# Kernel tuning notes

Hardware: AMD Instinct MI355X
Metric: run time of the kernel (lower is better)

Reference implementation:

```python
import jax, jax.numpy as jnp
import numpy as np

B, T = 4, 2048
IN_DIM = 128          # eff_in_dim == eff_out_dim (n_groups = 1)
IN_POINTS = 32
OUT_POINTS = 32
QUERY_DIM = 256
OUT_QUERY_DIM = 256
HIDDEN = QUERY_DIM // 4                       # 64
CHANNEL_PARAMS = IN_DIM * IN_DIM              # 16384
SPATIAL_PARAMS = OUT_POINTS * IN_POINTS       # 1024
TOTAL_PARAMS = CHANNEL_PARAMS + SPATIAL_PARAMS  # 17408
LN_EPS = 1e-6


def setup_inputs() -> dict:
    key = jax.random.key(0)
    ks = jax.random.split(key, 10)
    inp = {
        "sampled": jax.random.normal(ks[0], (B, T, 1, IN_POINTS, IN_DIM), jnp.float32),
        "query": jax.random.normal(ks[1], (B, T, QUERY_DIM), jnp.float32),
        # parameter_generator: LayerNorm(QUERY_DIM) -> Linear(QUERY_DIM, HIDDEN) -> Linear(HIDDEN, TOTAL_PARAMS)
        "ln_w": jnp.ones((QUERY_DIM,), jnp.float32) * QUERY_DIM ** -0.5,
        "ln_b": jnp.zeros((QUERY_DIM,), jnp.float32),
        "w1": jax.random.normal(ks[2], (HIDDEN, QUERY_DIM), jnp.float32) * 0.05,
        "b1": jax.random.normal(ks[3], (HIDDEN,), jnp.float32) * 0.02,
        "w2": jax.random.normal(ks[4], (TOTAL_PARAMS, HIDDEN), jnp.float32) * 0.05,
        "b2": jax.random.normal(ks[5], (TOTAL_PARAMS,), jnp.float32) * 0.05,
        "m_beta": jnp.zeros((IN_DIM,), jnp.float32),
        "s_beta": jnp.zeros((OUT_POINTS,), jnp.float32),
        "wo": jax.random.normal(ks[6], (OUT_QUERY_DIM, IN_DIM * OUT_POINTS), jnp.float32) * 0.02,
        "bo": jax.random.normal(ks[7], (OUT_QUERY_DIM,), jnp.float32) * 0.02,
    }
    return inp


def reference(sampled, query, ln_w, ln_b, w1, b1, w2, b2, m_beta, s_beta, wo, bo):
    b, t, g, P, C = sampled.shape  # g == 1
    BT = b * t
    OP = s_beta.shape[0]

    # parameter generator: LN -> Linear -> Linear (no activation in between)
    mu = jnp.mean(query, axis=-1, keepdims=True)
    var = jnp.var(query, axis=-1, keepdims=True)
    q = (query - mu) * jax.lax.rsqrt(var + LN_EPS) * ln_w + ln_b
    h = q @ w1.T + b1                               # [B, T, HIDDEN]
    params = (h @ w2.T + b2).reshape(BT, -1)        # [BT, TOTAL_PARAMS]

    channel_mixing = params[:, : C * C].reshape(BT, C, C)      # [BT, C, C]
    spatial_mixing = params[:, C * C :].reshape(BT, OP, P)     # [BT, OP, P]

    x = sampled.reshape(BT, P, C)
    # channel mixing: baddbmm(m_beta, x, channel_mixing) then GELU (exact/erf)
    x = jax.nn.gelu(jnp.einsum("bpc,bcd->bpd", x, channel_mixing) + m_beta,
                    approximate=False)
    # spatial mixing: baddbmm(s_beta, spatial_mixing, x) then GELU
    x = jax.nn.gelu(jnp.einsum("bop,bpd->bod", spatial_mixing, x) + s_beta[:, None],
                    approximate=False)

    out = x.reshape(b, t, -1) @ wo.T + bo           # [B, T, OUT_QUERY_DIM]
    return out
```

## Files before the change

kernel.cpp:

```cpp
#include <hip/hip_runtime.h>
#include <cstdint>


typedef __bf16 bf16x8 __attribute__((ext_vector_type(8)));
typedef float  f32x4  __attribute__((ext_vector_type(4)));
typedef unsigned short ushort;
typedef ushort ushort8 __attribute__((ext_vector_type(8)));

#define TW 16

__device__ __forceinline__ ushort f2b(float f) {
    union { float f; uint32_t u; } v; v.f = f;
    uint32_t u = v.u;
    u += 0x7fffu + ((u >> 16) & 1u);
    return (ushort)(u >> 16);
}
__device__ __forceinline__ uint32_t pk2(float a, float b) {
    return (uint32_t)f2b(a) | ((uint32_t)f2b(b) << 16);
}
__device__ __forceinline__ float gelu_fast(float x) {
    float z = fabsf(x) * 0.70710678118654752440f;
    float t = __builtin_amdgcn_rcpf(fmaf(0.3275911f, z, 1.0f));
    float p = t * fmaf(t, fmaf(t, fmaf(t, fmaf(t, 1.061405429f, -1.453152027f),
                                       1.421413741f), -0.284496736f), 0.254829592f);
    float e = __expf(-z * z);
    float erfv = copysignf(fmaf(-p, e, 1.0f), x);
    return 0.5f * x * (1.0f + erfv);
}

__global__ void prep(const float* __restrict__ w2, const float* __restrict__ w1,
                     const float* __restrict__ wo, const float* __restrict__ b2,
                     ushort* __restrict__ w2p, ushort* __restrict__ w2sp,
                     ushort* __restrict__ w1p, ushort* __restrict__ wop,
                     float* __restrict__ b2t) {
    int i = blockIdx.x * 256 + threadIdx.x;
    {
        int j = i & 7, l = (i >> 3) & 63, ks = (i >> 9) & 1;
        int d = (i >> 10) & 127, cb = (i >> 17) & 7;
        w2p[i] = f2b(w2[(size_t)((cb * 16 + (l & 15)) * 128 + d) * 64 +
                        ks * 32 + (l >> 4) * 8 + j]);
    }
    {
        int j = i & 7, l = (i >> 3) & 63, nb = (i >> 9) & 15, kc5 = (i >> 13) & 127;
        int o = (l >> 4) * 8 + j, q = nb * 16 + (l & 15);
        int d16 = kc5 & 15, dt2 = kc5 >> 4;
        wop[i] = f2b(wo[(size_t)q * 4096 + o * 128 + dt2 * 16 + d16]);
    }
    if (i < 65536) {
        int j = i & 7, l = (i >> 3) & 63, ks = (i >> 9) & 1, g = (i >> 10) & 63;
        w2sp[i] = f2b(w2[(size_t)(16384 + g * 16 + (l & 15)) * 64 +
                         ks * 32 + (l >> 4) * 8 + j]);
    }
    if (i < 16384) {
        int j = i & 7, l = (i >> 3) & 63, ks = (i >> 9) & 7, nb = i >> 12;
        w1p[i] = f2b(w1[(nb * 16 + (l & 15)) * 256 + ks * 32 + (l >> 4) * 8 + j]);
        b2t[i] = b2[(i & 127) * 128 + (i >> 7)];
    }
}

__launch_bounds__(512, 2)
__global__ void fused(const float* __restrict__ sampled, const float* __restrict__ query,
                      const float* __restrict__ ln_w, const float* __restrict__ ln_b,
                      const float* __restrict__ b1, const float* __restrict__ b2,
                      const float* __restrict__ m_beta, const float* __restrict__ s_beta,
                      const ushort* __restrict__ w2p, const ushort* __restrict__ w2sp,
                      const ushort* __restrict__ w1p, const float* __restrict__ b2t,
                      ushort* __restrict__ y2f) {
    __shared__ ushort Hb[TW * 64];
    __shared__ union {
        ushort qn[TW * 264];
        ushort smT[TW * 1032];
        struct {
            ushort pt[TW * 1032];
            ushort g1s[TW * 640];
        } mp;
    } U;
    __shared__ float mb_s[128];
    __shared__ float sb_s[32];

    const int tid  = threadIdx.x;
    const int wv   = tid >> 6;
    const int lane = tid & 63;
    const int lq   = lane >> 4;
    const int ln16 = lane & 15;
    const int tok0 = blockIdx.x * TW;

    if (tid < 128) mb_s[tid] = m_beta[tid];
    else if (tid < 160) sb_s[tid - 128] = s_beta[tid - 128];

    for (int tt = 0; tt < 2; ++tt) {
        int t = wv * 2 + tt;
        const float* q = query + (size_t)(tok0 + t) * 256;
        float2 a = *(const float2*)(q + 2 * lane);
        float2 b = *(const float2*)(q + 128 + 2 * lane);
        float s = a.x + a.y + b.x + b.y;
        for (int off = 1; off < 64; off <<= 1) s += __shfl_xor(s, off);
        float mu = s * (1.0f / 256.0f);
        float d0 = a.x - mu, d1 = a.y - mu, d2 = b.x - mu, d3 = b.y - mu;
        float ss = d0 * d0 + d1 * d1 + d2 * d2 + d3 * d3;
        for (int off = 1; off < 64; off <<= 1) ss += __shfl_xor(ss, off);
        float rstd = rsqrtf(ss * (1.0f / 256.0f) + 1e-6f);
        int i0 = 2 * lane, i1 = 2 * lane + 128;
        float q0 = d0 * rstd * ln_w[i0]     + ln_b[i0];
        float q1 = d1 * rstd * ln_w[i0 + 1] + ln_b[i0 + 1];
        float q2 = d2 * rstd * ln_w[i1]     + ln_b[i1];
        float q3 = d3 * rstd * ln_w[i1 + 1] + ln_b[i1 + 1];
        *(uint32_t*)&U.qn[t * 264 + i0] = pk2(q0, q1);
        *(uint32_t*)&U.qn[t * 264 + i1] = pk2(q2, q3);
    }
    __syncthreads();

    if (wv < 4) {
        int nb = wv;
        f32x4 acc = {0.0f, 0.0f, 0.0f, 0.0f};
        for (int ks = 0; ks < 8; ++ks) {
            bf16x8 afr = *(const bf16x8*)&U.qn[ln16 * 264 + ks * 32 + lq * 8];
            bf16x8 bfr = *(const bf16x8*)&w1p[(nb * 8 + ks) * 512 + lane * 8];
            acc = __builtin_amdgcn_mfma_f32_16x16x32_bf16(afr, bfr, acc, 0, 0, 0);
        }
        float bias = b1[nb * 16 + ln16];
        for (int i = 0; i < 4; ++i) {
            int t = lq * 4 + i;
            Hb[t * 64 + nb * 16 + ln16] = f2b(acc[i] + bias);
        }
    }
    __syncthreads();

    bf16x8 hfr[2];
    hfr[0] = *(const bf16x8*)&Hb[ln16 * 64 + 0 + lq * 8];
    hfr[1] = *(const bf16x8*)&Hb[ln16 * 64 + 32 + lq * 8];

    for (int gi = 0; gi < 8; ++gi) {
        int g = wv * 8 + gi;
        f32x4 acc = *(const f32x4*)&b2[16384 + g * 16 + lq * 4];
        for (int ks = 0; ks < 2; ++ks) {
            bf16x8 afr = *(const bf16x8*)&w2sp[(g * 2 + ks) * 512 + lane * 8];
            acc = __builtin_amdgcn_mfma_f32_16x16x32_bf16(afr, hfr[ks], acc, 0, 0, 0);
        }
        int o = g >> 1;
        int p0 = (g & 1) * 16 + lq * 4;
        uint2 wr;
        wr.x = pk2(acc[0], acc[1]);
        wr.y = pk2(acc[2], acc[3]);
        *(uint2*)&U.smT[ln16 * 1032 + o * 32 + p0] = wr;
    }

    bf16x8 xa[2][2][4];
    for (int tt = 0; tt < 2; ++tt) {
        const float* xp = sampled + (size_t)(tok0 + wv * 2 + tt) * 4096;
        for (int mt = 0; mt < 2; ++mt) {
            int p = mt * 16 + ln16;
            for (int ks = 0; ks < 4; ++ks) {
                int c = ks * 32 + lq * 8;
                float4 lo = *(const float4*)(xp + p * 128 + c);
                float4 hi = *(const float4*)(xp + p * 128 + c + 4);
                ushort8 u;
                u[0] = f2b(lo.x); u[1] = f2b(lo.y); u[2] = f2b(lo.z); u[3] = f2b(lo.w);
                u[4] = f2b(hi.x); u[5] = f2b(hi.y); u[6] = f2b(hi.z); u[7] = f2b(hi.w);
                xa[tt][mt][ks] = __builtin_bit_cast(bf16x8, u);
            }
        }
    }
    __syncthreads();

    bf16x8 sa[2][2];
    for (int tt = 0; tt < 2; ++tt) {
        int t = wv * 2 + tt;
        for (int mt = 0; mt < 2; ++mt)
            sa[tt][mt] = *(const bf16x8*)&U.smT[t * 1032 + (mt * 16 + ln16) * 32 + lq * 8];
    }
    __syncthreads();

    for (int dt = 0; dt < 16; ++dt) {
        const int cb = wv;
        for (int dd = 0; dd < 8; ++dd) {
            int d = dt * 8 + dd;
            f32x4 acc = *(const f32x4*)&b2t[d * 128 + cb * 16 + lq * 4];
            for (int ks = 0; ks < 2; ++ks) {
                bf16x8 afr = *(const bf16x8*)&w2p[((cb * 128 + d) * 2 + ks) * 512 + lane * 8];
                acc = __builtin_amdgcn_mfma_f32_16x16x32_bf16(afr, hfr[ks], acc, 0, 0, 0);
            }
            uint2 wr;
            wr.x = pk2(acc[0], acc[1]);
            wr.y = pk2(acc[2], acc[3]);
            *(uint2*)&U.mp.pt[ln16 * 1032 + ((cb * 2 + (lq >> 1)) * 8 + dd) * 8 + (lq & 1) * 4] = wr;
        }
        __syncthreads();

        const int ddl = ln16 & 7;
        for (int tt = 0; tt < 2; ++tt) {
            int t = wv * 2 + tt;
            bf16x8 bfr[4];
            for (int ks = 0; ks < 4; ++ks)
                bfr[ks] = *(const bf16x8*)&U.mp.pt[t * 1032 + (ks * 4 + lq) * 64 + ddl * 8];
            float mb = mb_s[dt * 8 + ddl];
            for (int mt = 0; mt < 2; ++mt) {
                f32x4 acc = {0.0f, 0.0f, 0.0f, 0.0f};
                for (int ks = 0; ks < 4; ++ks)
                    acc = __builtin_amdgcn_mfma_f32_16x16x32_bf16(xa[tt][mt][ks], bfr[ks], acc, 0, 0, 0);
                float g0 = gelu_fast(acc[0] + mb);
                float g1 = gelu_fast(acc[1] + mb);
                float g2 = gelu_fast(acc[2] + mb);
                float g3 = gelu_fast(acc[3] + mb);
                if (ln16 < 8) {
                    uint2 wr;
                    wr.x = pk2(g0, g1);
                    wr.y = pk2(g2, g3);
                    *(uint2*)&U.mp.g1s[t * 640 + ((dt & 1) * 8 + ddl) * 40 + mt * 16 + lq * 4] = wr;
                }
            }
        }

        if (dt & 1) {
            __builtin_amdgcn_wave_barrier();
            int dt2 = dt >> 1;
            for (int tt = 0; tt < 2; ++tt) {
                int t = wv * 2 + tt;
                bf16x8 gb = *(const bf16x8*)&U.mp.g1s[t * 640 + ln16 * 40 + lq * 8];
                for (int mt = 0; mt < 2; ++mt) {
                    f32x4 acc = {0.0f, 0.0f, 0.0f, 0.0f};
                    acc = __builtin_amdgcn_mfma_f32_16x16x32_bf16(sa[tt][mt], gb, acc, 0, 0, 0);
                    float4 sbv = *(const float4*)&sb_s[mt * 16 + lq * 4];
                    float g0 = gelu_fast(acc[0] + sbv.x);
                    float g1 = gelu_fast(acc[1] + sbv.y);
                    float g2 = gelu_fast(acc[2] + sbv.z);
                    float g3 = gelu_fast(acc[3] + sbv.w);
                    uint2 wr;
                    wr.x = pk2(g0, g1);
                    wr.y = pk2(g2, g3);
                    size_t addr = (size_t)blockIdx.x * 65536 +
                                  (dt2 * 16 + ln16) * 512 +
                                  (t + (mt * 2 + (lq >> 1)) * 16) * 8 + (lq & 1) * 4;
                    *(uint2*)&y2f[addr] = wr;
                }
            }
        }
        __syncthreads();
    }
}

__launch_bounds__(512, 2)
__global__ void outproj(const ushort* __restrict__ y2f, const ushort* __restrict__ wop,
                        const float* __restrict__ bo, float* __restrict__ out) {
    __shared__ float red[32 * 264];
    const int tid  = threadIdx.x;
    const int wv   = tid >> 6;
    const int lane = tid & 63;
    const int lq   = lane >> 4;
    const int ln16 = lane & 15;
    const int tb   = blockIdx.x;

    f32x4 acc[2][16];
    for (int m = 0; m < 2; ++m)
        for (int nb = 0; nb < 16; ++nb) acc[m][nb] = (f32x4){0.0f, 0.0f, 0.0f, 0.0f};

    const ushort* ap0 = y2f + ((size_t)(tb * 2 + 0) * 128 + wv * 16) * 512 + lane * 8;
    const ushort* ap1 = y2f + ((size_t)(tb * 2 + 1) * 128 + wv * 16) * 512 + lane * 8;
    const ushort* bp  = wop + (size_t)(wv * 16) * 8192 + lane * 8;
    for (int it = 0; it < 16; ++it) {
        bf16x8 a0 = *(const bf16x8*)(ap0 + it * 512);
        bf16x8 a1 = *(const bf16x8*)(ap1 + it * 512);
        for (int nb = 0; nb < 16; ++nb) {
            bf16x8 bf = *(const bf16x8*)(bp + (it * 16 + nb) * 512);
            acc[0][nb] = __builtin_amdgcn_mfma_f32_16x16x32_bf16(a0, bf, acc[0][nb], 0, 0, 0);
            acc[1][nb] = __builtin_amdgcn_mfma_f32_16x16x32_bf16(a1, bf, acc[1][nb], 0, 0, 0);
        }
    }

    for (int w = 0; w < 8; ++w) {
        if (wv == w) {
            for (int m = 0; m < 2; ++m)
                for (int nb = 0; nb < 16; ++nb)
                    for (int i = 0; i < 4; ++i) {
                        float* p = &red[(m * 16 + lq * 4 + i) * 264 + nb * 16 + ln16];
                        if (w == 0) *p = acc[m][nb][i];
                        else        *p += acc[m][nb][i];
                    }
        }
        __syncthreads();
    }

    int r  = tid >> 4;
    int q0 = (tid & 15) * 16;
    float* op = out + (size_t)(tb * 32 + r) * 256 + q0;
    for (int c = 0; c < 16; c += 4) {
        float4 a = *(const float4*)&red[r * 264 + q0 + c];
        float4 b = *(const float4*)&bo[q0 + c];
        float4 o = {a.x + b.x, a.y + b.y, a.z + b.z, a.w + b.w};
        *(float4*)(op + c) = o;
    }
}

extern "C" void kernel_launch(void* const* d_in, const int* in_sizes, int n_in,
                              void* d_out, int out_size, void* d_ws, size_t ws_size,
                              hipStream_t stream) {
    const float* sampled = (const float*)d_in[0];
    const float* query   = (const float*)d_in[1];
    const float* ln_w    = (const float*)d_in[2];
    const float* ln_b    = (const float*)d_in[3];
    const float* w1      = (const float*)d_in[4];
    const float* b1      = (const float*)d_in[5];
    const float* w2      = (const float*)d_in[6];
    const float* b2      = (const float*)d_in[7];
    const float* m_beta  = (const float*)d_in[8];
    const float* s_beta  = (const float*)d_in[9];
    const float* wo      = (const float*)d_in[10];
    const float* bo      = (const float*)d_in[11];
    float* out = (float*)d_out;

    char* ws = (char*)d_ws;
    ushort* w2p  = (ushort*)(ws);
    ushort* wop  = (ushort*)(ws + 2097152);
    ushort* w2sp = (ushort*)(ws + 4194304);
    ushort* w1p  = (ushort*)(ws + 4325376);
    float*  b2t  = (float*) (ws + 4358144);
    ushort* y2f  = (ushort*)(ws + 4423680);

    prep<<<4096, 256, 0, stream>>>(w2, w1, wo, b2, w2p, w2sp, w1p, wop, b2t);
    fused<<<512, 512, 0, stream>>>(sampled, query, ln_w, ln_b, b1, b2,
                                   m_beta, s_beta, w2p, w2sp, w1p, b2t, y2f);
    outproj<<<256, 512, 0, stream>>>(y2f, wop, bo, out);
}
```

Measured before the change: 450.8 us.

## Split outproj over output columns per wave and halve GELU work in channel mix

The output projection now gives each wave its own slice of output columns and runs the full K loop. This removes the cross-wave split-K reduction through shared memory and its eight serialized barriers, but every wave now reads the whole activation row block from global memory. In the channel-mixing stage, all 16 lanes now each compute GELU on two values instead of four, with the upper half of the lanes handling the upper accumulator pair. Previously half the lanes computed four GELUs and then discarded them.

```diff
diff --git a/kernel.cpp b/kernel.cpp
--- a/kernel.cpp
+++ b/kernel.cpp
@@ -188,6 +188,7 @@
         __syncthreads();
 
         const int ddl = ln16 & 7;
+        const bool hi = ln16 >= 8;
         for (int tt = 0; tt < 2; ++tt) {
             int t = wv * 2 + tt;
             bf16x8 bfr[4];
@@ -198,16 +199,12 @@
                 f32x4 acc = {0.0f, 0.0f, 0.0f, 0.0f};
                 for (int ks = 0; ks < 4; ++ks)
                     acc = __builtin_amdgcn_mfma_f32_16x16x32_bf16(xa[tt][mt][ks], bfr[ks], acc, 0, 0, 0);
-                float g0 = gelu_fast(acc[0] + mb);
-                float g1 = gelu_fast(acc[1] + mb);
-                float g2 = gelu_fast(acc[2] + mb);
-                float g3 = gelu_fast(acc[3] + mb);
-                if (ln16 < 8) {
-                    uint2 wr;
-                    wr.x = pk2(g0, g1);
-                    wr.y = pk2(g2, g3);
-                    *(uint2*)&U.mp.g1s[t * 640 + ((dt & 1) * 8 + ddl) * 40 + mt * 16 + lq * 4] = wr;
-                }
+                float va = hi ? acc[2] : acc[0];
+                float vb = hi ? acc[3] : acc[1];
+                float ga = gelu_fast(va + mb);
+                float gb = gelu_fast(vb + mb);
+                int p = mt * 16 + lq * 4 + (hi ? 2 : 0);
+                *(uint32_t*)&U.mp.g1s[t * 640 + ((dt & 1) * 8 + ddl) * 40 + p] = pk2(ga, gb);
             }
         }
 
@@ -242,7 +239,6 @@
 __launch_bounds__(512, 2)
 __global__ void outproj(const ushort* __restrict__ y2f, const ushort* __restrict__ wop,
                         const float* __restrict__ bo, float* __restrict__ out) {
-    __shared__ float red[32 * 264];
     const int tid  = threadIdx.x;
     const int wv   = tid >> 6;
     const int lane = tid & 63;
@@ -250,44 +246,34 @@
     const int ln16 = lane & 15;
     const int tb   = blockIdx.x;
 
-    f32x4 acc[2][16];
+    f32x4 acc[2][2];
     for (int m = 0; m < 2; ++m)
-        for (int nb = 0; nb < 16; ++nb) acc[m][nb] = (f32x4){0.0f, 0.0f, 0.0f, 0.0f};
-
-    const ushort* ap0 = y2f + ((size_t)(tb * 2 + 0) * 128 + wv * 16) * 512 + lane * 8;
-    const ushort* ap1 = y2f + ((size_t)(tb * 2 + 1) * 128 + wv * 16) * 512 + lane * 8;
-    const ushort* bp  = wop + (size_t)(wv * 16) * 8192 + lane * 8;
-    for (int it = 0; it < 16; ++it) {
-        bf16x8 a0 = *(const bf16x8*)(ap0 + it * 512);
-        bf16x8 a1 = *(const bf16x8*)(ap1 + it * 512);
-        for (int nb = 0; nb < 16; ++nb) {
-            bf16x8 bf = *(const bf16x8*)(bp + (it * 16 + nb) * 512);
-            acc[0][nb] = __builtin_amdgcn_mfma_f32_16x16x32_bf16(a0, bf, acc[0][nb], 0, 0, 0);
-            acc[1][nb] = __builtin_amdgcn_mfma_f32_16x16x32_bf16(a1, bf, acc[1][nb], 0, 0, 0);
-        }
-    }
-
-    for (int w = 0; w < 8; ++w) {
-        if (wv == w) {
-            for (int m = 0; m < 2; ++m)
-                for (int nb = 0; nb < 16; ++nb)
-                    for (int i = 0; i < 4; ++i) {
-                        float* p = &red[(m * 16 + lq * 4 + i) * 264 + nb * 16 + ln16];
-                        if (w == 0) *p = acc[m][nb][i];
-                        else        *p += acc[m][nb][i];
-                    }
-        }
-        __syncthreads();
-    }
-
-    int r  = tid >> 4;
-    int q0 = (tid & 15) * 16;
-    float* op = out + (size_t)(tb * 32 + r) * 256 + q0;
-    for (int c = 0; c < 16; c += 4) {
-        float4 a = *(const float4*)&red[r * 264 + q0 + c];
-        float4 b = *(const float4*)&bo[q0 + c];
-        float4 o = {a.x + b.x, a.y + b.y, a.z + b.z, a.w + b.w};
-        *(float4*)(op + c) = o;
+        for (int n = 0; n < 2; ++n) acc[m][n] = (f32x4){0.0f, 0.0f, 0.0f, 0.0f};
+
+    const ushort* a0 = y2f + (size_t)(tb * 2) * 65536 + lane * 8;
+    const ushort* a1 = a0 + 65536;
+    const ushort* bp = wop + (size_t)(wv * 2) * 512 + lane * 8;
+
+    #pragma unroll 4
+    for (int k = 0; k < 128; ++k) {
+        bf16x8 af0 = *(const bf16x8*)(a0 + k * 512);
+        bf16x8 af1 = *(const bf16x8*)(a1 + k * 512);
+        bf16x8 bf0 = *(const bf16x8*)(bp + (size_t)k * 8192);
+        bf16x8 bf1 = *(const bf16x8*)(bp + (size_t)k * 8192 + 512);
+        acc[0][0] = __builtin_amdgcn_mfma_f32_16x16x32_bf16(af0, bf0, acc[0][0], 0, 0, 0);
+        acc[0][1] = __builtin_amdgcn_mfma_f32_16x16x32_bf16(af0, bf1, acc[0][1], 0, 0, 0);
+        acc[1][0] = __builtin_amdgcn_mfma_f32_16x16x32_bf16(af1, bf0, acc[1][0], 0, 0, 0);
+        acc[1][1] = __builtin_amdgcn_mfma_f32_16x16x32_bf16(af1, bf1, acc[1][1], 0, 0, 0);
+    }
+
+    for (int n = 0; n < 2; ++n) {
+        int q = (wv * 2 + n) * 16 + ln16;
+        float bov = bo[q];
+        for (int m = 0; m < 2; ++m)
+            for (int i = 0; i < 4; ++i) {
+                int tok = tb * 32 + m * 16 + lq * 4 + i;
+                out[(size_t)tok * 256 + q] = acc[m][n][i] + bov;
+            }
     }
 }
 
```

After: 387.7 us. 14.0% less time.
